# Kernel tuning notes

Hardware: AMD Instinct MI355X
Metric: run time of the kernel (lower is better)

The kernel has to match this reference:

```python
import jax, jax.numpy as jnp
import numpy as np

B, T, D_MODEL = 2, 2048, 2048
NH, NKV, DH = 16, 4, 128
N_REP = NH // NKV
NV = 256  # n_vision_tokens
THETA = 10000.0
NEG = -1e9


def setup_inputs() -> dict:
    key = jax.random.key(0)
    ks = jax.random.split(key, 5)
    x = jax.random.normal(ks[0], (B, T, D_MODEL), jnp.float32)
    # rope_freqs = exp(i * t * theta^{-2j/D}) represented as cos/sin, shape [T, DH//2]
    inv = 1.0 / (THETA ** (np.arange(0, DH, 2, dtype=np.float64) / DH))
    ang = np.outer(np.arange(T, dtype=np.float64), inv)
    cos = jnp.asarray(np.cos(ang), jnp.float32)
    sin = jnp.asarray(np.sin(ang), jnp.float32)
    sc = 0.02
    wq = jax.random.normal(ks[1], (D_MODEL, NH * DH), jnp.float32) * sc
    wk = jax.random.normal(ks[2], (D_MODEL, NKV * DH), jnp.float32) * sc
    wv = jax.random.normal(ks[3], (D_MODEL, NKV * DH), jnp.float32) * sc
    wo = jax.random.normal(ks[4], (NH * DH, D_MODEL), jnp.float32) * sc
    return {"x": x, "cos": cos, "sin": sin, "wq": wq, "wk": wk, "wv": wv,
            "wo": wo, "n_vision_tokens": NV}


def _rope(t, cos, sin):
    # t: [B,H,L,D]; pairs (even=real, odd=imag); cos/sin: [L, D//2]
    a = t[..., 0::2]
    b = t[..., 1::2]
    c = cos[None, None]
    s = sin[None, None]
    ra = a * c - b * s
    rb = a * s + b * c
    return jnp.stack([ra, rb], axis=-1).reshape(t.shape)


def reference(x, cos, sin, wq, wk, wv, wo, n_vision_tokens):
    Bx, Tx, _ = x.shape
    nv = int(n_vision_tokens)
    tl = Tx - nv  # text length

    q = (x @ wq).reshape(Bx, Tx, NH, DH).transpose(0, 2, 1, 3)   # [B,NH,T,DH]
    k = (x @ wk).reshape(Bx, Tx, NKV, DH).transpose(0, 2, 1, 3)  # [B,NKV,T,DH]
    v = (x @ wv).reshape(Bx, Tx, NKV, DH).transpose(0, 2, 1, 3)

    # RoPE only on the text portion (vision tokens keep raw q/k)
    c, s = cos[:tl], sin[:tl]
    q = jnp.concatenate([q[:, :, :nv], _rope(q[:, :, nv:], c, s)], axis=2)
    k = jnp.concatenate([k[:, :, :nv], _rope(k[:, :, nv:], c, s)], axis=2)

    new_kv_cache = (k, v)

    # GQA: repeat_interleave KV heads
    k = jnp.repeat(k, N_REP, axis=1)
    v = jnp.repeat(v, N_REP, axis=1)

    attn = jnp.einsum('bhqd,bhkd->bhqk', q, k) / jnp.sqrt(jnp.float32(DH))

    # hybrid mask: vision rows/cols fully visible; text-text strictly causal
    text_mask = jnp.triu(jnp.ones((tl, tl), bool), k=1)
    mask = jnp.zeros((Tx, Tx), bool).at[nv:, nv:].set(text_mask)
    attn = jnp.where(mask[None, None], NEG, attn)

    attn = jax.nn.softmax(attn, axis=-1)
    out = jnp.einsum('bhqk,bhkd->bhqd', attn, v)
    out = out.transpose(0, 2, 1, 3).reshape(Bx, Tx, NH * DH) @ wo
    return out, new_kv_cache
```

## Files before the change

### kernel.cpp

```cpp
#include <hip/hip_runtime.h>
#include <hip/hip_bf16.h>

#define BB 2
#define TT 2048
#define DMODEL 2048
#define NH 16
#define NKV 4
#define DH 128
#define NV 256
#define TL (TT - NV)
#define NQKV 3072

typedef __bf16  bf16x8  __attribute__((ext_vector_type(8)));
typedef float   float4v __attribute__((ext_vector_type(4)));
typedef short   short8  __attribute__((ext_vector_type(8)));
typedef unsigned short ushort;

__device__ __forceinline__ float bf2f(ushort u) {
    union { float f; unsigned i; } c; c.i = ((unsigned)u) << 16; return c.f;
}
__device__ __forceinline__ ushort f2bf(float f) {
    union { float f; unsigned i; } c; c.f = f;
    unsigned r = c.i + 0x7fff + ((c.i >> 16) & 1);
    return (ushort)(r >> 16);
}
__device__ __forceinline__ unsigned cvtpk(float a, float b) {
    unsigned r;
    asm("v_cvt_pk_bf16_f32 %0, %1, %2" : "=v"(r) : "v"(a), "v"(b));
    return r;
}

#define GLDS16(g, l) __builtin_amdgcn_global_load_lds( \
    (__attribute__((address_space(1))) void*)(g), \
    (__attribute__((address_space(3))) void*)(l), 16, 0, 0)

#define NJOB 51
#define NSLOT 19
#define WOJOBS 64
__device__ const short J_QT[NJOB] = {
    16,  0, 0, 1, 1, 2, 2, 3, 3, 31, 31, 30, 15,
    30, 29, 29, 28, 14, 28, 27, 27, 26, 13, 26, 25, 25, 24, 12,
    24, 23, 23, 22, 11, 22, 21, 21, 20, 10, 20, 19, 19, 18,  9,
    18, 17, 17,  8,  7,  6,  5,  4 };
__device__ const short J_K0[NJOB] = {
     0,  0,16, 0,16, 0,16, 0,16,  0, 16,  0,  0,
    16,  0,15, 0,  0, 15,  0, 14,  0,  0, 14,  0, 13,  0,  0,
    13,  0,12, 0,  0, 12,  0, 11,  0,  0, 11,  0, 10,  0,  0,
    10,  0, 9, 0,  0,  0,  0,  0 };
__device__ const short J_K1[NJOB] = {
    17, 16,32,16,32,16,32,16,32, 16, 32, 16, 16,
    31, 15,30,15, 15, 29, 14, 28, 14, 14, 27, 13, 26, 13, 13,
    25, 12,24,12, 12, 23, 11, 22, 11, 11, 21, 10, 20, 10, 10,
    19,  9,18, 9,  8,  7,  6,  5 };
__device__ const short J_PH[NJOB] = {
   255,  0, 1, 2, 3, 4, 5, 6, 7, 36, 37, 34,255,
    35, 32,33,30,255, 31, 28, 29, 26,255, 27, 24, 25, 22,255,
    23, 20,21,18,255, 19, 16, 17, 14,255, 15, 12, 13, 10,255,
    11,  8, 9,255,255,255,255,255 };

__global__ __launch_bounds__(256) void prep(
    const float* __restrict__ x, ushort* __restrict__ xbf,
    const float* __restrict__ wq, const float* __restrict__ wk,
    const float* __restrict__ wv, ushort* __restrict__ wT)
{
    __shared__ ushort st[64][72];
    int bid = blockIdx.x;
    if (bid < 4096) {
        size_t i = ((size_t)bid * 256 + threadIdx.x) * 8;
        float4v f0 = *(const float4v*)&x[i];
        float4v f1 = *(const float4v*)&x[i + 4];
        short8 h;
        h[0] = (short)f2bf(f0[0]); h[1] = (short)f2bf(f0[1]);
        h[2] = (short)f2bf(f0[2]); h[3] = (short)f2bf(f0[3]);
        h[4] = (short)f2bf(f1[0]); h[5] = (short)f2bf(f1[1]);
        h[6] = (short)f2bf(f1[2]); h[7] = (short)f2bf(f1[3]);
        *(short8*)&xbf[i] = h;
        return;
    }
    bid -= 4096;
    int bx = bid % 48, by = bid / 48;
    int n0 = bx * 64, k0 = by * 64;
    const float* w; int N, nn;
    if (n0 < 2048)      { w = wq; N = 2048; nn = n0; }
    else if (n0 < 2560) { w = wk; N = 512;  nn = n0 - 2048; }
    else                { w = wv; N = 512;  nn = n0 - 2560; }
    int r  = threadIdx.x >> 2;
    int c0 = (threadIdx.x & 3) * 16;
    #pragma unroll
    for (int j = 0; j < 16; j += 4) {
        float4v f = *(const float4v*)&w[(size_t)(k0 + r) * N + nn + c0 + j];
        st[c0 + j + 0][r] = f2bf(f[0]);
        st[c0 + j + 1][r] = f2bf(f[1]);
        st[c0 + j + 2][r] = f2bf(f[2]);
        st[c0 + j + 3][r] = f2bf(f[3]);
    }
    __syncthreads();
    ushort* dst = &wT[(size_t)(n0 + r) * DMODEL + k0];
    *(short8*)&dst[c0]     = *(short8*)&st[r][c0];
    *(short8*)&dst[c0 + 8] = *(short8*)&st[r][c0 + 8];
}

#define RQ_BLOCKS 14336
#define RK_BLOCKS 4096
__global__ __launch_bounds__(256) void postproc(
    ushort* __restrict__ qkv,
    const float* __restrict__ cosp, const float* __restrict__ sinp,
    float* __restrict__ kout, float* __restrict__ vout,
    ushort* __restrict__ kbf, ushort* __restrict__ vbfT)
{
    __shared__ ushort st[64][72];
    int bid = blockIdx.x;
    if (bid < RQ_BLOCKS) {
        int b   = bid / (RQ_BLOCKS / 2);
        int idx = (bid % (RQ_BLOCKS / 2)) * 256 + threadIdx.x;
        int i  = idx & 63;
        int h  = (idx >> 6) & 15;
        int tr = idx >> 10;
        int t  = NV + tr;
        size_t off = ((size_t)(b * TT + t)) * NQKV + h * DH + 2 * i;
        unsigned pk = *(const unsigned*)&qkv[off];
        float a  = bf2f((ushort)(pk & 0xffff));
        float bb = bf2f((ushort)(pk >> 16));
        float c  = cosp[tr * 64 + i];
        float s  = sinp[tr * 64 + i];
        *(unsigned*)&qkv[off] = cvtpk(a * c - bb * s, a * s + bb * c);
        return;
    }
    bid -= RQ_BLOCKS;
    if (bid < RK_BLOCKS) {
        int idx = bid * 256 + threadIdx.x;
        int i  = idx & 63;
        int kh = (idx >> 6) & 3;
        int t  = (idx >> 8) & 2047;
        int b  = idx >> 19;
        size_t row = ((size_t)(b * TT + t)) * NQKV;
        size_t dst = ((size_t)((b * NKV + kh) * TT + t)) * DH + 2 * i;
        unsigned pk = *(const unsigned*)&qkv[row + 2048 + kh * DH + 2 * i];
        float ka = bf2f((ushort)(pk & 0xffff));
        float kb = bf2f((ushort)(pk >> 16));
        if (t >= NV) {
            int pos = t - NV;
            float c = cosp[pos * 64 + i];
            float s = sinp[pos * 64 + i];
            float ra = ka * c - kb * s;
            float rb = ka * s + kb * c;
            ka = ra; kb = rb;
        }
        kout[dst]     = ka;
        kout[dst + 1] = kb;
        *(unsigned*)&kbf[dst] = cvtpk(ka, kb);
        unsigned pv = *(const unsigned*)&qkv[row + 2560 + kh * DH + 2 * i];
        vout[dst]     = bf2f((ushort)(pv & 0xffff));
        vout[dst + 1] = bf2f((ushort)(pv >> 16));
        return;
    }
    bid -= RK_BLOCKS;
    {
        int bx = bid & 31, by = (bid >> 5) & 1, bk = bid >> 6;
        int t0 = bx * 64, d0 = by * 64;
        int b = bk >> 2, kh = bk & 3;
        int r  = threadIdx.x >> 2;
        int c0 = (threadIdx.x & 3) * 16;
        const ushort* src = qkv + ((size_t)(b * TT + t0 + r)) * NQKV + 2560 + kh * DH + d0;
        short8 a0 = *(const short8*)&src[c0];
        short8 a1 = *(const short8*)&src[c0 + 8];
        #pragma unroll
        for (int j = 0; j < 8; j++) {
            st[c0 + j][r]     = (ushort)a0[j];
            st[c0 + 8 + j][r] = (ushort)a1[j];
        }
        __syncthreads();
        ushort* dst = vbfT + ((size_t)(bk * DH + d0 + r)) * TT + t0;
        *(short8*)&dst[c0]     = *(short8*)&st[r][c0];
        *(short8*)&dst[c0 + 8] = *(short8*)&st[r][c0 + 8];
    }
}

__global__ __launch_bounds__(256) void gemm_lds(
    const ushort* __restrict__ A, int lda,
    const ushort* __restrict__ BT,
    ushort* __restrict__ C, int ldc, int K)
{
    __shared__ ushort As[2][128 * 32];
    __shared__ ushort Bs[2][128 * 32];

    int tid = threadIdx.x;
    int wave = tid >> 6, lane = tid & 63, quad = lane >> 4, l16 = lane & 15;

    int nwg = gridDim.x * gridDim.y;
    int bid = blockIdx.x + gridDim.x * blockIdx.y;
    int cpx = nwg >> 3;
    int swz = (bid & 7) * cpx + (bid >> 3);
    int bx = swz % gridDim.x, by = swz / gridDim.x;
    int m0 = by * 128, n0 = bx * 128;
    int wr = (wave >> 1) * 64, wc = (wave & 1) * 64;

    int srow = tid >> 2, scol = (tid & 3) * 8;
    const ushort* ag = A  + (size_t)(m0 + srow) * lda + scol;
    const ushort* bg = BT + (size_t)(n0 + srow) * K   + scol;
    int lo0 = (wave * 16) * 32;
    int lo1 = (64 + wave * 16) * 32;

    float4v acc[4][4];
    for (int i = 0; i < 4; i++)
        for (int j = 0; j < 4; j++)
            acc[i][j] = (float4v){0.f, 0.f, 0.f, 0.f};

    auto stage = [&](int buf, int k0) {
        GLDS16(ag + k0,                    As[buf] + lo0);
        GLDS16(ag + (size_t)64 * lda + k0, As[buf] + lo1);
        GLDS16(bg + k0,                    Bs[buf] + lo0);
        GLDS16(bg + (size_t)64 * K + k0,   Bs[buf] + lo1);
    };

    stage(0, 0);
    int it = 0;
    for (int k0 = 0; k0 < K; k0 += 32, ++it) {
        int cur = it & 1;
        __syncthreads();
        if (k0 + 32 < K) stage(cur ^ 1, k0 + 32);

        bf16x8 af[4], bfr[4];
        #pragma unroll
        for (int i = 0; i < 4; i++) af[i] = *(const bf16x8*)&As[cur][(wr + i * 16 + l16) * 32 + quad * 8];
        #pragma unroll
        for (int j = 0; j < 4; j++) bfr[j] = *(const bf16x8*)&Bs[cur][(wc + j * 16 + l16) * 32 + quad * 8];
        #pragma unroll
        for (int i = 0; i < 4; i++)
            #pragma unroll
            for (int j = 0; j < 4; j++)
                acc[i][j] = __builtin_amdgcn_mfma_f32_16x16x32_bf16(af[i], bfr[j], acc[i][j], 0, 0, 0);
    }

    #pragma unroll
    for (int i = 0; i < 4; i++)
        #pragma unroll
        for (int j = 0; j < 4; j++)
            #pragma unroll
            for (int r = 0; r < 4; r++) {
                int row = m0 + wr + i * 16 + quad * 4 + r;
                int col = n0 + wc + j * 16 + l16;
                C[(size_t)row * ldc + col] = f2bf(acc[i][j][r]);
            }
}

__global__ __launch_bounds__(256) void gemm_out(
    const ushort* __restrict__ A,
    const ushort* __restrict__ Bc,
    float* __restrict__ C)
{
    __shared__ ushort As[2][128 * 32];
    __shared__ ushort Bs[2][128 * 32];

    int tid = threadIdx.x;
    int wave = tid >> 6, lane = tid & 63, quad = lane >> 4, l16 = lane & 15;

    int nwg = gridDim.x * gridDim.y;
    int bid = blockIdx.x + gridDim.x * blockIdx.y;
    int cpx = nwg >> 3;
    int swz = (bid & 7) * cpx + (bid >> 3);
    int bx = swz % gridDim.x, by = swz / gridDim.x;
    int m0 = by * 128, n0 = bx * 128;
    int wr = (wave >> 1) * 64, wc = (wave & 1) * 64;

    int srow = tid >> 2, scol = (tid & 3) * 8;
    const ushort* ag = A  + (size_t)(m0 + srow) * NQKV + scol;
    const ushort* bg = Bc + (size_t)(n0 + srow) * 6144 + scol;
    int lo0 = (wave * 16) * 32;
    int lo1 = (64 + wave * 16) * 32;

    float4v acc[4][4];
    for (int i = 0; i < 4; i++)
        for (int j = 0; j < 4; j++)
            acc[i][j] = (float4v){0.f, 0.f, 0.f, 0.f};

    auto stage = [&](int buf, int k0) {
        int koff = ((k0 >> 10) * NQKV) + (k0 & 1023);
        GLDS16(ag + k0,                       As[buf] + lo0);
        GLDS16(ag + (size_t)64 * NQKV + k0,   As[buf] + lo1);
        GLDS16(bg + koff,                     Bs[buf] + lo0);
        GLDS16(bg + (size_t)64 * 6144 + koff, Bs[buf] + lo1);
    };

    stage(0, 0);
    int it = 0;
    for (int k0 = 0; k0 < 2048; k0 += 32, ++it) {
        int cur = it & 1;
        __syncthreads();
        if (k0 + 32 < 2048) stage(cur ^ 1, k0 + 32);

        bf16x8 af[4], bfr[4];
        #pragma unroll
        for (int i = 0; i < 4; i++) af[i] = *(const bf16x8*)&As[cur][(wr + i * 16 + l16) * 32 + quad * 8];
        #pragma unroll
        for (int j = 0; j < 4; j++) bfr[j] = *(const bf16x8*)&Bs[cur][(wc + j * 16 + l16) * 32 + quad * 8];
        #pragma unroll
        for (int i = 0; i < 4; i++)
            #pragma unroll
            for (int j = 0; j < 4; j++)
                acc[i][j] = __builtin_amdgcn_mfma_f32_16x16x32_bf16(af[i], bfr[j], acc[i][j], 0, 0, 0);
    }

    #pragma unroll
    for (int i = 0; i < 4; i++)
        #pragma unroll
        for (int j = 0; j < 4; j++)
            #pragma unroll
            for (int r = 0; r < 4; r++) {
                int row = m0 + wr + i * 16 + quad * 4 + r;
                int col = n0 + wc + j * 16 + l16;
                C[(size_t)row * DMODEL + col] = acc[i][j][r];
            }
}

__global__ __launch_bounds__(256, 2) void attn_kernel(
    ushort* qkv,
    const ushort* __restrict__ kbf, const ushort* __restrict__ vbfT,
    ushort* __restrict__ pO, float* __restrict__ ml,
    const float* __restrict__ wo)
{
    __shared__ ushort shm[40960];

    int tid = threadIdx.x;
    int hy = blockIdx.x;
    int b  = blockIdx.y;
    int zz = blockIdx.z;

    if (zz >= NJOB) {
        int idx = (zz - NJOB) * 16 + b * 8 + hy;
        int n0 = (idx & 31) * 64, k0 = (idx >> 5) * 64;
        ushort (*st)[72] = (ushort(*)[72])shm;
        int r  = tid >> 2;
        int c0 = (tid & 3) * 16;
        #pragma unroll
        for (int j = 0; j < 16; j += 4) {
            float4v f = *(const float4v*)&wo[(size_t)(k0 + r) * DMODEL + n0 + c0 + j];
            st[c0 + j + 0][r] = f2bf(f[0]);
            st[c0 + j + 1][r] = f2bf(f[1]);
            st[c0 + j + 2][r] = f2bf(f[2]);
            st[c0 + j + 3][r] = f2bf(f[3]);
        }
        __syncthreads();
        ushort* dst = qkv + ((size_t)(2 * (n0 + r) + (k0 >> 10))) * NQKV + 2048 + (k0 & 1023);
        *(short8*)&dst[c0]     = *(short8*)&st[r][c0];
        *(short8*)&dst[c0 + 8] = *(short8*)&st[r][c0 + 8];
        return;
    }

    int job = zz;
    int wave = tid >> 6, lane = tid & 63, quad = lane >> 4, l16 = lane & 15;
    int qt  = J_QT[job];
    int kt0 = J_K0[job];
    int kt1 = J_K1[job];
    int ph  = J_PH[job];
    int h0 = hy * 2;
    int kh = hy >> 1;
    int q0 = qt * 64;

    int srow = tid >> 2, scol = (tid & 3) * 8;

    ushort* qbase0 = qkv + ((size_t)(b * TT) + q0) * NQKV + h0 * DH;
    ushort* qbase1 = qbase0 + DH;
    #pragma unroll
    for (int dk = 0; dk < 4; dk++) {
        GLDS16(qbase0 + (size_t)srow * NQKV + dk * 32 + scol, shm + dk * 2048 + wave * 512);
        GLDS16(qbase1 + (size_t)srow * NQKV + dk * 32 + scol, shm + 16384 + dk * 2048 + wave * 512);
    }
    __syncthreads();
    bf16x8 qf0[4], qf1[4];
    #pragma unroll
    for (int dk = 0; dk < 4; dk++) {
        qf0[dk] = *(const bf16x8*)&shm[dk * 2048 + (wave * 16 + l16) * 32 + quad * 8];
        qf1[dk] = *(const bf16x8*)&shm[16384 + dk * 2048 + (wave * 16 + l16) * 32 + quad * 8];
    }
    __syncthreads();

    float4v O0[8], O1[8];
    #pragma unroll
    for (int i = 0; i < 8; i++) {
        O0[i] = (float4v){0.f, 0.f, 0.f, 0.f};
        O1[i] = (float4v){0.f, 0.f, 0.f, 0.f};
    }
    float m0r = -1e30f, l0r = 0.f;
    float m1r = -1e30f, l1r = 0.f;

    const float scale = 0.08838834764831845f;
    const float THRR  = 90.50966799f;
    int qg = q0 + wave * 16 + l16;

    const ushort* kb2 = kbf  + ((size_t)(b * NKV + kh)) * TT * DH;
    const ushort* vb2 = vbfT + ((size_t)(b * NKV + kh)) * DH * TT;

    ushort* Pl = shm + 32768 + wave * 2048;
    int qsw = l16 & 7;

    auto stage = [&](int buf, int kt) {
        ushort* Kb = shm + buf * 16384;
        ushort* Vb = Kb + 8192;
        int k0 = kt * 64;
        #pragma unroll
        for (int dk = 0; dk < 4; dk++)
            GLDS16(kb2 + (size_t)(k0 + srow) * DH + dk * 32 + scol, Kb + dk * 2048 + wave * 512);
        #pragma unroll
        for (int kk = 0; kk < 2; kk++)
            #pragma unroll
            for (int p = 0; p < 2; p++)
                GLDS16(vb2 + (size_t)(p * 64 + srow) * TT + k0 + kk * 32 + scol,
                       Vb + kk * 4096 + (p * 64 + wave * 16) * 32);
    };

    stage(0, kt0);

    for (int kt = kt0; kt < kt1; kt++) {
        int cur = (kt - kt0) & 1;
        __syncthreads();
        if (kt + 1 < kt1)
            stage(cur ^ 1, kt + 1);

        const ushort* Kc = shm + cur * 16384;
        const ushort* Vc = Kc + 8192;
        int k0 = kt * 64;

        float4v s0[4], s1[4];
        __builtin_amdgcn_s_setprio(1);
        #pragma unroll
        for (int t2i = 0; t2i < 4; t2i++) {
            float4v a0 = (float4v){0.f, 0.f, 0.f, 0.f};
            float4v a1 = (float4v){0.f, 0.f, 0.f, 0.f};
            #pragma unroll
            for (int dk = 0; dk < 4; dk++) {
                bf16x8 af = *(const bf16x8*)&Kc[dk * 2048 + (t2i * 16 + l16) * 32 + quad * 8];
                a0 = __builtin_amdgcn_mfma_f32_16x16x32_bf16(af, qf0[dk], a0, 0, 0, 0);
                a1 = __builtin_amdgcn_mfma_f32_16x16x32_bf16(af, qf1[dk], a1, 0, 0, 0);
            }
            s0[t2i] = a0; s1[t2i] = a1;
        }
        __builtin_amdgcn_s_setprio(0);

        if ((q0 >= NV) && (kt == qt)) {
            #pragma unroll
            for (int t2i = 0; t2i < 4; t2i++)
                #pragma unroll
                for (int i = 0; i < 4; i++)
                    if (k0 + t2i * 16 + quad * 4 + i > qg) {
                        s0[t2i][i] = -1e9f;
                        s1[t2i][i] = -1e9f;
                    }
        }

        float mx0 = -1e30f, mx1 = -1e30f;
        #pragma unroll
        for (int t2i = 0; t2i < 4; t2i++)
            #pragma unroll
            for (int i = 0; i < 4; i++) {
                mx0 = fmaxf(mx0, s0[t2i][i]);
                mx1 = fmaxf(mx1, s1[t2i][i]);
            }
        mx0 = fmaxf(mx0, __shfl_xor(mx0, 16, 64));
        mx0 = fmaxf(mx0, __shfl_xor(mx0, 32, 64));
        mx1 = fmaxf(mx1, __shfl_xor(mx1, 16, 64));
        mx1 = fmaxf(mx1, __shfl_xor(mx1, 32, 64));

        bool skip0 = __all(mx0 <= m0r + THRR);
        bool skip1 = __all(mx1 <= m1r + THRR);
        float mn0 = fmaxf(m0r, mx0), mn1 = fmaxf(m1r, mx1);
        float mref0 = skip0 ? m0r : mn0;
        float mref1 = skip1 ? m1r : mn1;
        float nb0 = -mref0 * scale;
        float nb1 = -mref1 * scale;

        float ss0 = 0.f, ss1 = 0.f;
        #pragma unroll
        for (int t2i = 0; t2i < 4; t2i++)
            #pragma unroll
            for (int i = 0; i < 4; i++) {
                float p0 = __expf(__builtin_fmaf(s0[t2i][i], scale, nb0)); s0[t2i][i] = p0; ss0 += p0;
                float p1 = __expf(__builtin_fmaf(s1[t2i][i], scale, nb1)); s1[t2i][i] = p1; ss1 += p1;
            }
        ss0 += __shfl_xor(ss0, 16, 64); ss0 += __shfl_xor(ss0, 32, 64);
        ss1 += __shfl_xor(ss1, 16, 64); ss1 += __shfl_xor(ss1, 32, 64);

        if (!skip0) {
            float al0 = __expf((m0r - mn0) * scale);
            #pragma unroll
            for (int dt = 0; dt < 8; dt++)
                #pragma unroll
                for (int i = 0; i < 4; i++) O0[dt][i] *= al0;
            l0r *= al0;
            m0r = mn0;
        }
        l0r += ss0;
        if (!skip1) {
            float al1 = __expf((m1r - mn1) * scale);
            #pragma unroll
            for (int dt = 0; dt < 8; dt++)
                #pragma unroll
                for (int i = 0; i < 4; i++) O1[dt][i] *= al1;
            l1r *= al1;
            m1r = mn1;
        }
        l1r += ss1;

        #pragma unroll
        for (int t2i = 0; t2i < 4; t2i++) {
            int g = t2i * 2 + (quad >> 1);
            int base = l16 * 64 + ((g ^ qsw) << 3) + (quad & 1) * 4;
            *(unsigned*)&Pl[base]            = cvtpk(s0[t2i][0], s0[t2i][1]);
            *(unsigned*)&Pl[base + 2]        = cvtpk(s0[t2i][2], s0[t2i][3]);
            *(unsigned*)&Pl[1024 + base]     = cvtpk(s1[t2i][0], s1[t2i][1]);
            *(unsigned*)&Pl[1024 + base + 2] = cvtpk(s1[t2i][2], s1[t2i][3]);
        }

        #pragma unroll
        for (int kk = 0; kk < 2; kk++) {
            int gc = kk * 4 + quad;
            int raddr = l16 * 64 + ((gc ^ qsw) << 3);
            bf16x8 pf0 = *(const bf16x8*)&Pl[raddr];
            bf16x8 pf1 = *(const bf16x8*)&Pl[1024 + raddr];
            __builtin_amdgcn_s_setprio(1);
            #pragma unroll
            for (int dt = 0; dt < 8; dt++) {
                bf16x8 vf = *(const bf16x8*)&Vc[kk * 4096 + (dt * 16 + l16) * 32 + quad * 8];
                O0[dt] = __builtin_amdgcn_mfma_f32_16x16x32_bf16(vf, pf0, O0[dt], 0, 0, 0);
                O1[dt] = __builtin_amdgcn_mfma_f32_16x16x32_bf16(vf, pf1, O1[dt], 0, 0, 0);
            }
            __builtin_amdgcn_s_setprio(0);
        }
    }

    float rinv0 = 1.f / l0r, rinv1 = 1.f / l1r;
    int qrow = wave * 16 + l16;
    if (ph == 255 || (ph & 1)) {
        size_t orow = (size_t)qrow * NQKV;
        #pragma unroll
        for (int dt = 0; dt < 8; dt++)
            #pragma unroll
            for (int i = 0; i < 4; i += 2) {
                unsigned pk0 = cvtpk(O0[dt][i] * rinv0, O0[dt][i + 1] * rinv0);
                unsigned pk1 = cvtpk(O1[dt][i] * rinv1, O1[dt][i + 1] * rinv1);
                *(unsigned*)&qbase0[orow + dt * 16 + quad * 4 + i] = pk0;
                *(unsigned*)&qbase1[orow + dt * 16 + quad * 4 + i] = pk1;
            }
    } else {
        int g = ((b * 8 + hy) * NSLOT) + (ph >> 1);
        ushort* pb = pO + (size_t)g * 16384 + qrow * 256;
        #pragma unroll
        for (int dt = 0; dt < 8; dt++)
            #pragma unroll
            for (int i = 0; i < 4; i += 2) {
                int d = dt * 16 + quad * 4 + i;
                *(unsigned*)&pb[d]       = cvtpk(O0[dt][i] * rinv0, O0[dt][i + 1] * rinv0);
                *(unsigned*)&pb[128 + d] = cvtpk(O1[dt][i] * rinv1, O1[dt][i + 1] * rinv1);
            }
    }
    if (ph != 255 && quad == 0) {
        int g = ((b * 8 + hy) * NSLOT) + (ph >> 1);
        int half = ph & 1;
        float* mlb = ml + (size_t)g * 512 + half * 256 + qrow * 2;
        mlb[0]   = m0r;  mlb[1]   = l0r;
        mlb[128] = m1r;  mlb[129] = l1r;
    }
}

__global__ __launch_bounds__(256) void combine_split(
    ushort* __restrict__ qkv, const ushort* __restrict__ pO,
    const float* __restrict__ ml)
{
    int g = blockIdx.x;
    int slice = g / NSLOT, local = g % NSLOT;
    int b = slice >> 3, hy = slice & 7;
    int qt = (local < 4) ? local : (13 + local);
    int h0 = hy * 2;
    int q0 = qt * 64;

    int t = threadIdx.x;
    int r = t >> 2, seg = t & 3;
    int head = seg >> 1;
    const float scale = 0.08838834764831845f;

    const float* mlg = ml + (size_t)g * 512;
    float m0 = mlg[0 * 256 + head * 128 + r * 2];
    float l0 = mlg[0 * 256 + head * 128 + r * 2 + 1];
    float m1 = mlg[1 * 256 + head * 128 + r * 2];
    float l1 = mlg[1 * 256 + head * 128 + r * 2 + 1];
    float mm = fmaxf(m0, m1);
    float w0 = __expf((m0 - mm) * scale) * l0;
    float w1 = __expf((m1 - mm) * scale) * l1;
    float inv = 1.f / (w0 + w1);
    float a0 = w0 * inv, a1 = w1 * inv;

    const ushort* p = pO + (size_t)g * 16384 + r * 256 + seg * 64;
    ushort* q = qkv + ((size_t)(b * TT + q0 + r)) * NQKV + (h0 + head) * DH + (seg & 1) * 64;

    #pragma unroll
    for (int j = 0; j < 64; j += 2) {
        unsigned u0 = *(const unsigned*)&p[j];
        unsigned u1 = *(const unsigned*)&q[j];
        float lo = bf2f((ushort)(u0 & 0xffff)) * a0 + bf2f((ushort)(u1 & 0xffff)) * a1;
        float hi2 = bf2f((ushort)(u0 >> 16)) * a0 + bf2f((ushort)(u1 >> 16)) * a1;
        *(unsigned*)&q[j] = cvtpk(lo, hi2);
    }
}

extern "C" void kernel_launch(void* const* d_in, const int* in_sizes, int n_in,
                              void* d_out, int out_size, void* d_ws, size_t ws_size,
                              hipStream_t stream) {
    const float* x    = (const float*)d_in[0];
    const float* cosp = (const float*)d_in[1];
    const float* sinp = (const float*)d_in[2];
    const float* wq   = (const float*)d_in[3];
    const float* wk   = (const float*)d_in[4];
    const float* wv   = (const float*)d_in[5];
    const float* wo   = (const float*)d_in[6];

    float* out  = (float*)d_out;
    float* kout = out + (size_t)BB * TT * DMODEL;
    float* vout = kout + (size_t)BB * NKV * TT * DH;

    ushort* sc    = (ushort*)d_out;
    ushort* wqkvT = sc;
    ushort* xbf   = sc + (size_t)NQKV * DMODEL;
    ushort* kbf   = sc + (size_t)NQKV * DMODEL;
    ushort* vbfT  = kbf + (size_t)BB * NKV * TT * DH;
    ushort* pO    = sc;
    float*  ml    = (float*)(sc + 15000000);

    ushort* qkv = (ushort*)d_ws;

    const int M = BB * TT;

    prep<<<dim3(4096 + 1536), 256, 0, stream>>>(x, xbf, wq, wk, wv, wqkvT);

    gemm_lds<<<dim3(NQKV / 128, M / 128), 256, 0, stream>>>(
        xbf, DMODEL, wqkvT, qkv, NQKV, DMODEL);

    postproc<<<dim3(RQ_BLOCKS + RK_BLOCKS + 512), 256, 0, stream>>>(
        qkv, cosp, sinp, kout, vout, kbf, vbfT);

    attn_kernel<<<dim3(NH / 2, BB, NJOB + WOJOBS), 256, 0, stream>>>(
        qkv, kbf, vbfT, pO, ml, wo);

    combine_split<<<dim3(16 * NSLOT), 256, 0, stream>>>(qkv, pO, ml);

    gemm_out<<<dim3(DMODEL / 128, M / 128), 256, 0, stream>>>(qkv, qkv + 2048, out);
}
```

Baseline: 342.7 us.

## Process all four GQA query heads per block sharing K/V tiles, vectorize postproc

The attention kernel now uses 512-thread blocks that cover all four query heads of one KV head. Each K/V tile staged in LDS is therefore reused by 8 waves instead of 4, which halves K/V global traffic. The split-K job schedule, the partial-output and ml layouts, and the combine kernel are reworked to match, and the Wo transpose jobs are packed two per block. The postproc RoPE and K/V conversion paths now handle 8 elements per thread with vector loads and stores. The trade-offs are fewer blocks, a higher register and occupancy target (launch bounds of 512 threads, 4 blocks), and more LDS traffic for the P matrix.

```diff
diff --git a/kernel.cpp b/kernel.cpp
--- a/kernel.cpp
+++ b/kernel.cpp
@@ -34,29 +34,29 @@
     (__attribute__((address_space(1))) void*)(g), \
     (__attribute__((address_space(3))) void*)(l), 16, 0, 0)
 
-#define NJOB 51
-#define NSLOT 19
+#define NJOB 52
+#define NSLOT 20
 #define WOJOBS 64
 __device__ const short J_QT[NJOB] = {
-    16,  0, 0, 1, 1, 2, 2, 3, 3, 31, 31, 30, 15,
-    30, 29, 29, 28, 14, 28, 27, 27, 26, 13, 26, 25, 25, 24, 12,
-    24, 23, 23, 22, 11, 22, 21, 21, 20, 10, 20, 19, 19, 18,  9,
-    18, 17, 17,  8,  7,  6,  5,  4 };
+     0,  0,  1,  1,  2,  2,  3,  3, 30, 31, 31, 15,
+    28, 29, 29, 30, 14, 26, 27, 27, 28, 13, 24, 25, 25, 26, 12,
+    22, 23, 23, 24, 11, 20, 21, 21, 22, 10, 18, 19, 19, 20,  9,
+    16, 17, 17, 18,  8, 16,  7,  6,  5,  4 };
 __device__ const short J_K0[NJOB] = {
-     0,  0,16, 0,16, 0,16, 0,16,  0, 16,  0,  0,
-    16,  0,15, 0,  0, 15,  0, 14,  0,  0, 14,  0, 13,  0,  0,
-    13,  0,12, 0,  0, 12,  0, 11,  0,  0, 11,  0, 10,  0,  0,
-    10,  0, 9, 0,  0,  0,  0,  0 };
+     0, 16,  0, 16,  0, 16,  0, 16, 15,  0, 16,  0,
+    14,  0, 15,  0,  0, 13,  0, 14,  0,  0, 12,  0, 13,  0,  0,
+    11,  0, 12,  0,  0, 10,  0, 11,  0,  0,  9,  0, 10,  0,  0,
+     8,  0,  9,  0,  0,  0,  0,  0,  0,  0 };
 __device__ const short J_K1[NJOB] = {
-    17, 16,32,16,32,16,32,16,32, 16, 32, 16, 16,
-    31, 15,30,15, 15, 29, 14, 28, 14, 14, 27, 13, 26, 13, 13,
-    25, 12,24,12, 12, 23, 11, 22, 11, 11, 21, 10, 20, 10, 10,
-    19,  9,18, 9,  8,  7,  6,  5 };
+    16, 32, 16, 32, 16, 32, 16, 32, 31, 16, 32, 16,
+    29, 15, 30, 15, 15, 27, 14, 28, 14, 14, 25, 13, 26, 13, 13,
+    23, 12, 24, 12, 12, 21, 11, 22, 11, 11, 19, 10, 20, 10, 10,
+    17,  9, 18,  9,  9,  8,  8,  7,  6,  5 };
 __device__ const short J_PH[NJOB] = {
-   255,  0, 1, 2, 3, 4, 5, 6, 7, 36, 37, 34,255,
-    35, 32,33,30,255, 31, 28, 29, 26,255, 27, 24, 25, 22,255,
-    23, 20,21,18,255, 19, 16, 17, 14,255, 15, 12, 13, 10,255,
-    11,  8, 9,255,255,255,255,255 };
+     0,  1,  2,  3,  4,  5,  6,  7, 37, 38, 39, 255,
+    33, 34, 35, 36, 255, 29, 30, 31, 32, 255, 25, 26, 27, 28, 255,
+    21, 22, 23, 24, 255, 17, 18, 19, 20, 255, 13, 14, 15, 16, 255,
+     9, 10, 11, 12, 255,  8, 255, 255, 255, 255 };
 
 __global__ __launch_bounds__(256) void prep(
     const float* __restrict__ x, ushort* __restrict__ xbf,
@@ -100,8 +100,8 @@
     *(short8*)&dst[c0 + 8] = *(short8*)&st[r][c0 + 8];
 }
 
-#define RQ_BLOCKS 14336
-#define RK_BLOCKS 4096
+#define RQ_BLOCKS 3584
+#define RK_BLOCKS 1024
 __global__ __launch_bounds__(256) void postproc(
     ushort* __restrict__ qkv,
     const float* __restrict__ cosp, const float* __restrict__ sinp,
@@ -111,47 +111,69 @@
     __shared__ ushort st[64][72];
     int bid = blockIdx.x;
     if (bid < RQ_BLOCKS) {
-        int b   = bid / (RQ_BLOCKS / 2);
-        int idx = (bid % (RQ_BLOCKS / 2)) * 256 + threadIdx.x;
-        int i  = idx & 63;
-        int h  = (idx >> 6) & 15;
-        int tr = idx >> 10;
-        int t  = NV + tr;
-        size_t off = ((size_t)(b * TT + t)) * NQKV + h * DH + 2 * i;
-        unsigned pk = *(const unsigned*)&qkv[off];
-        float a  = bf2f((ushort)(pk & 0xffff));
-        float bb = bf2f((ushort)(pk >> 16));
-        float c  = cosp[tr * 64 + i];
-        float s  = sinp[tr * 64 + i];
-        *(unsigned*)&qkv[off] = cvtpk(a * c - bb * s, a * s + bb * c);
+        int idx = bid * 256 + threadIdx.x;
+        int i4 = idx & 15;
+        int h  = (idx >> 4) & 15;
+        int tr = idx >> 8;
+        int b  = tr >= TL;
+        int trr = tr - b * TL;
+        size_t off = ((size_t)(b * TT + NV + trr)) * NQKV + h * DH + i4 * 8;
+        short8 v = *(const short8*)&qkv[off];
+        float4v c4 = *(const float4v*)&cosp[trr * 64 + i4 * 4];
+        float4v s4 = *(const float4v*)&sinp[trr * 64 + i4 * 4];
+        short8 o;
+        #pragma unroll
+        for (int p = 0; p < 4; p++) {
+            float a  = bf2f((ushort)v[2 * p]);
+            float bb = bf2f((ushort)v[2 * p + 1]);
+            unsigned pk = cvtpk(a * c4[p] - bb * s4[p], a * s4[p] + bb * c4[p]);
+            o[2 * p]     = (short)(pk & 0xffff);
+            o[2 * p + 1] = (short)(pk >> 16);
+        }
+        *(short8*)&qkv[off] = o;
         return;
     }
     bid -= RQ_BLOCKS;
     if (bid < RK_BLOCKS) {
         int idx = bid * 256 + threadIdx.x;
-        int i  = idx & 63;
-        int kh = (idx >> 6) & 3;
-        int t  = (idx >> 8) & 2047;
-        int b  = idx >> 19;
+        int i4 = idx & 15;
+        int kh = (idx >> 4) & 3;
+        int t  = (idx >> 6) & 2047;
+        int b  = idx >> 17;
         size_t row = ((size_t)(b * TT + t)) * NQKV;
-        size_t dst = ((size_t)((b * NKV + kh) * TT + t)) * DH + 2 * i;
-        unsigned pk = *(const unsigned*)&qkv[row + 2048 + kh * DH + 2 * i];
-        float ka = bf2f((ushort)(pk & 0xffff));
-        float kb = bf2f((ushort)(pk >> 16));
+        size_t dst = ((size_t)((b * NKV + kh) * TT + t)) * DH + i4 * 8;
+        short8 kv = *(const short8*)&qkv[row + 2048 + kh * DH + i4 * 8];
+        short8 vv = *(const short8*)&qkv[row + 2560 + kh * DH + i4 * 8];
+        float kf[8];
+        #pragma unroll
+        for (int p = 0; p < 8; p++) kf[p] = bf2f((ushort)kv[p]);
         if (t >= NV) {
             int pos = t - NV;
-            float c = cosp[pos * 64 + i];
-            float s = sinp[pos * 64 + i];
-            float ra = ka * c - kb * s;
-            float rb = ka * s + kb * c;
-            ka = ra; kb = rb;
-        }
-        kout[dst]     = ka;
-        kout[dst + 1] = kb;
-        *(unsigned*)&kbf[dst] = cvtpk(ka, kb);
-        unsigned pv = *(const unsigned*)&qkv[row + 2560 + kh * DH + 2 * i];
-        vout[dst]     = bf2f((ushort)(pv & 0xffff));
-        vout[dst + 1] = bf2f((ushort)(pv >> 16));
+            float4v c4 = *(const float4v*)&cosp[pos * 64 + i4 * 4];
+            float4v s4 = *(const float4v*)&sinp[pos * 64 + i4 * 4];
+            #pragma unroll
+            for (int p = 0; p < 4; p++) {
+                float ra = kf[2 * p] * c4[p] - kf[2 * p + 1] * s4[p];
+                float rb = kf[2 * p] * s4[p] + kf[2 * p + 1] * c4[p];
+                kf[2 * p] = ra; kf[2 * p + 1] = rb;
+            }
+        }
+        float4v ko0 = {kf[0], kf[1], kf[2], kf[3]};
+        float4v ko1 = {kf[4], kf[5], kf[6], kf[7]};
+        *(float4v*)&kout[dst]     = ko0;
+        *(float4v*)&kout[dst + 4] = ko1;
+        short8 kb8;
+        #pragma unroll
+        for (int p = 0; p < 4; p++) {
+            unsigned pk = cvtpk(kf[2 * p], kf[2 * p + 1]);
+            kb8[2 * p]     = (short)(pk & 0xffff);
+            kb8[2 * p + 1] = (short)(pk >> 16);
+        }
+        *(short8*)&kbf[dst] = kb8;
+        float4v vo0 = {bf2f((ushort)vv[0]), bf2f((ushort)vv[1]), bf2f((ushort)vv[2]), bf2f((ushort)vv[3])};
+        float4v vo1 = {bf2f((ushort)vv[4]), bf2f((ushort)vv[5]), bf2f((ushort)vv[6]), bf2f((ushort)vv[7])};
+        *(float4v*)&vout[dst]     = vo0;
+        *(float4v*)&vout[dst + 4] = vo1;
         return;
     }
     bid -= RK_BLOCKS;
@@ -313,7 +335,7 @@
             }
 }
 
-__global__ __launch_bounds__(256, 2) void attn_kernel(
+__global__ __launch_bounds__(512, 4) void attn_kernel(
     ushort* qkv,
     const ushort* __restrict__ kbf, const ushort* __restrict__ vbfT,
     ushort* __restrict__ pO, float* __restrict__ ml,
@@ -322,16 +344,16 @@
     __shared__ ushort shm[40960];
 
     int tid = threadIdx.x;
-    int hy = blockIdx.x;
-    int b  = blockIdx.y;
-    int zz = blockIdx.z;
+    int kh = blockIdx.x >> 1, b = blockIdx.x & 1;
+    int zz = blockIdx.y;
 
     if (zz >= NJOB) {
-        int idx = (zz - NJOB) * 16 + b * 8 + hy;
+        int half = tid >> 8, tid2 = tid & 255;
+        int idx = (zz - NJOB) * 16 + blockIdx.x * 2 + half;
         int n0 = (idx & 31) * 64, k0 = (idx >> 5) * 64;
-        ushort (*st)[72] = (ushort(*)[72])shm;
-        int r  = tid >> 2;
-        int c0 = (tid & 3) * 16;
+        ushort (*st)[72] = (ushort(*)[72])(shm + half * 4608);
+        int r  = tid2 >> 2;
+        int c0 = (tid2 & 3) * 16;
         #pragma unroll
         for (int j = 0; j < 16; j += 4) {
             float4v f = *(const float4v*)&wo[(size_t)(k0 + r) * DMODEL + n0 + c0 + j];
@@ -349,29 +371,29 @@
 
     int job = zz;
     int wave = tid >> 6, lane = tid & 63, quad = lane >> 4, l16 = lane & 15;
+    int pair = wave >> 2, wv = wave & 3;
     int qt  = J_QT[job];
     int kt0 = J_K0[job];
     int kt1 = J_K1[job];
     int ph  = J_PH[job];
-    int h0 = hy * 2;
-    int kh = hy >> 1;
     int q0 = qt * 64;
 
-    int srow = tid >> 2, scol = (tid & 3) * 8;
-
-    ushort* qbase0 = qkv + ((size_t)(b * TT) + q0) * NQKV + h0 * DH;
-    ushort* qbase1 = qbase0 + DH;
+    int lr = lane >> 2, lc = (lane & 3) * 8;
+
     #pragma unroll
-    for (int dk = 0; dk < 4; dk++) {
-        GLDS16(qbase0 + (size_t)srow * NQKV + dk * 32 + scol, shm + dk * 2048 + wave * 512);
-        GLDS16(qbase1 + (size_t)srow * NQKV + dk * 32 + scol, shm + 16384 + dk * 2048 + wave * 512);
+    for (int j = 0; j < 8; j++) {
+        int t = wave * 8 + j;
+        int g = t >> 4, r = t & 15, dk = r >> 2, rg = r & 3;
+        const ushort* qb = qkv + ((size_t)(b * TT) + q0 + rg * 16 + lr) * NQKV
+                         + (kh * 4 + g) * DH + dk * 32 + lc;
+        GLDS16(qb, shm + g * 8192 + dk * 2048 + rg * 512);
     }
     __syncthreads();
     bf16x8 qf0[4], qf1[4];
     #pragma unroll
     for (int dk = 0; dk < 4; dk++) {
-        qf0[dk] = *(const bf16x8*)&shm[dk * 2048 + (wave * 16 + l16) * 32 + quad * 8];
-        qf1[dk] = *(const bf16x8*)&shm[16384 + dk * 2048 + (wave * 16 + l16) * 32 + quad * 8];
+        qf0[dk] = *(const bf16x8*)&shm[(pair * 2 + 0) * 8192 + dk * 2048 + (wv * 16 + l16) * 32 + quad * 8];
+        qf1[dk] = *(const bf16x8*)&shm[(pair * 2 + 1) * 8192 + dk * 2048 + (wv * 16 + l16) * 32 + quad * 8];
     }
     __syncthreads();
 
@@ -386,12 +408,12 @@
 
     const float scale = 0.08838834764831845f;
     const float THRR  = 90.50966799f;
-    int qg = q0 + wave * 16 + l16;
+    int qg = q0 + wv * 16 + l16;
 
     const ushort* kb2 = kbf  + ((size_t)(b * NKV + kh)) * TT * DH;
     const ushort* vb2 = vbfT + ((size_t)(b * NKV + kh)) * DH * TT;
 
-    ushort* Pl = shm + 32768 + wave * 2048;
+    ushort* Pl = shm + 32768 + wave * 1024;
     int qsw = l16 & 7;
 
     auto stage = [&](int buf, int kt) {
@@ -399,14 +421,19 @@
         ushort* Vb = Kb + 8192;
         int k0 = kt * 64;
         #pragma unroll
-        for (int dk = 0; dk < 4; dk++)
-            GLDS16(kb2 + (size_t)(k0 + srow) * DH + dk * 32 + scol, Kb + dk * 2048 + wave * 512);
-        #pragma unroll
-        for (int kk = 0; kk < 2; kk++)
-            #pragma unroll
-            for (int p = 0; p < 2; p++)
-                GLDS16(vb2 + (size_t)(p * 64 + srow) * TT + k0 + kk * 32 + scol,
-                       Vb + kk * 4096 + (p * 64 + wave * 16) * 32);
+        for (int j = 0; j < 4; j++) {
+            int t = wave * 4 + j;
+            if (t < 16) {
+                int dk = t >> 2, rg = t & 3;
+                GLDS16(kb2 + (size_t)(k0 + rg * 16 + lr) * DH + dk * 32 + lc,
+                       Kb + dk * 2048 + rg * 512);
+            } else {
+                int t2 = t - 16;
+                int kk = t2 >> 3, p2 = (t2 >> 2) & 1, rg = t2 & 3;
+                GLDS16(vb2 + (size_t)(p2 * 64 + rg * 16 + lr) * TT + k0 + kk * 32 + lc,
+                       Vb + kk * 4096 + p2 * 2048 + rg * 512);
+            }
+        }
     };
 
     stage(0, kt0);
@@ -501,35 +528,49 @@
         }
         l1r += ss1;
 
+        bf16x8 pf0[2], pf1[2];
         #pragma unroll
         for (int t2i = 0; t2i < 4; t2i++) {
             int g = t2i * 2 + (quad >> 1);
             int base = l16 * 64 + ((g ^ qsw) << 3) + (quad & 1) * 4;
-            *(unsigned*)&Pl[base]            = cvtpk(s0[t2i][0], s0[t2i][1]);
-            *(unsigned*)&Pl[base + 2]        = cvtpk(s0[t2i][2], s0[t2i][3]);
-            *(unsigned*)&Pl[1024 + base]     = cvtpk(s1[t2i][0], s1[t2i][1]);
-            *(unsigned*)&Pl[1024 + base + 2] = cvtpk(s1[t2i][2], s1[t2i][3]);
-        }
-
+            *(unsigned*)&Pl[base]     = cvtpk(s0[t2i][0], s0[t2i][1]);
+            *(unsigned*)&Pl[base + 2] = cvtpk(s0[t2i][2], s0[t2i][3]);
+        }
         #pragma unroll
         for (int kk = 0; kk < 2; kk++) {
             int gc = kk * 4 + quad;
-            int raddr = l16 * 64 + ((gc ^ qsw) << 3);
-            bf16x8 pf0 = *(const bf16x8*)&Pl[raddr];
-            bf16x8 pf1 = *(const bf16x8*)&Pl[1024 + raddr];
+            pf0[kk] = *(const bf16x8*)&Pl[l16 * 64 + ((gc ^ qsw) << 3)];
+        }
+        #pragma unroll
+        for (int t2i = 0; t2i < 4; t2i++) {
+            int g = t2i * 2 + (quad >> 1);
+            int base = l16 * 64 + ((g ^ qsw) << 3) + (quad & 1) * 4;
+            *(unsigned*)&Pl[base]     = cvtpk(s1[t2i][0], s1[t2i][1]);
+            *(unsigned*)&Pl[base + 2] = cvtpk(s1[t2i][2], s1[t2i][3]);
+        }
+        #pragma unroll
+        for (int kk = 0; kk < 2; kk++) {
+            int gc = kk * 4 + quad;
+            pf1[kk] = *(const bf16x8*)&Pl[l16 * 64 + ((gc ^ qsw) << 3)];
+        }
+
+        #pragma unroll
+        for (int kk = 0; kk < 2; kk++) {
             __builtin_amdgcn_s_setprio(1);
             #pragma unroll
             for (int dt = 0; dt < 8; dt++) {
                 bf16x8 vf = *(const bf16x8*)&Vc[kk * 4096 + (dt * 16 + l16) * 32 + quad * 8];
-                O0[dt] = __builtin_amdgcn_mfma_f32_16x16x32_bf16(vf, pf0, O0[dt], 0, 0, 0);
-                O1[dt] = __builtin_amdgcn_mfma_f32_16x16x32_bf16(vf, pf1, O1[dt], 0, 0, 0);
+                O0[dt] = __builtin_amdgcn_mfma_f32_16x16x32_bf16(vf, pf0[kk], O0[dt], 0, 0, 0);
+                O1[dt] = __builtin_amdgcn_mfma_f32_16x16x32_bf16(vf, pf1[kk], O1[dt], 0, 0, 0);
             }
             __builtin_amdgcn_s_setprio(0);
         }
     }
 
     float rinv0 = 1.f / l0r, rinv1 = 1.f / l1r;
-    int qrow = wave * 16 + l16;
+    int qrow = wv * 16 + l16;
+    ushort* qbase0 = qkv + ((size_t)(b * TT) + q0) * NQKV + (kh * 4 + pair * 2) * DH;
+    ushort* qbase1 = qbase0 + DH;
     if (ph == 255 || (ph & 1)) {
         size_t orow = (size_t)qrow * NQKV;
         #pragma unroll
@@ -542,8 +583,8 @@
                 *(unsigned*)&qbase1[orow + dt * 16 + quad * 4 + i] = pk1;
             }
     } else {
-        int g = ((b * 8 + hy) * NSLOT) + (ph >> 1);
-        ushort* pb = pO + (size_t)g * 16384 + qrow * 256;
+        int g = ((b * 4 + kh) * NSLOT) + (ph >> 1);
+        ushort* pb = pO + (size_t)g * 32768 + qrow * 512 + (pair * 2) * 128;
         #pragma unroll
         for (int dt = 0; dt < 8; dt++)
             #pragma unroll
@@ -554,9 +595,9 @@
             }
     }
     if (ph != 255 && quad == 0) {
-        int g = ((b * 8 + hy) * NSLOT) + (ph >> 1);
-        int half = ph & 1;
-        float* mlb = ml + (size_t)g * 512 + half * 256 + qrow * 2;
+        int g = ((b * 4 + kh) * NSLOT) + (ph >> 1);
+        int part = ph & 1;
+        float* mlb = ml + (size_t)g * 1024 + part * 512 + (pair * 2) * 128 + qrow * 2;
         mlb[0]   = m0r;  mlb[1]   = l0r;
         mlb[128] = m1r;  mlb[129] = l1r;
     }
@@ -567,37 +608,35 @@
     const float* __restrict__ ml)
 {
     int g = blockIdx.x;
-    int slice = g / NSLOT, local = g % NSLOT;
-    int b = slice >> 3, hy = slice & 7;
-    int qt = (local < 4) ? local : (13 + local);
-    int h0 = hy * 2;
+    int slice = g / NSLOT, slot = g % NSLOT;
+    int b = slice >> 2, kh = slice & 3;
+    int qt = (slot < 4) ? slot : (slot + 12);
     int q0 = qt * 64;
 
     int t = threadIdx.x;
-    int r = t >> 2, seg = t & 3;
-    int head = seg >> 1;
+    int r = t >> 2, hh = t & 3;
     const float scale = 0.08838834764831845f;
 
-    const float* mlg = ml + (size_t)g * 512;
-    float m0 = mlg[0 * 256 + head * 128 + r * 2];
-    float l0 = mlg[0 * 256 + head * 128 + r * 2 + 1];
-    float m1 = mlg[1 * 256 + head * 128 + r * 2];
-    float l1 = mlg[1 * 256 + head * 128 + r * 2 + 1];
+    const float* mlg = ml + (size_t)g * 1024;
+    float m0 = mlg[hh * 128 + r * 2];
+    float l0 = mlg[hh * 128 + r * 2 + 1];
+    float m1 = mlg[512 + hh * 128 + r * 2];
+    float l1 = mlg[512 + hh * 128 + r * 2 + 1];
     float mm = fmaxf(m0, m1);
     float w0 = __expf((m0 - mm) * scale) * l0;
     float w1 = __expf((m1 - mm) * scale) * l1;
     float inv = 1.f / (w0 + w1);
     float a0 = w0 * inv, a1 = w1 * inv;
 
-    const ushort* p = pO + (size_t)g * 16384 + r * 256 + seg * 64;
-    ushort* q = qkv + ((size_t)(b * TT + q0 + r)) * NQKV + (h0 + head) * DH + (seg & 1) * 64;
+    const ushort* p = pO + (size_t)g * 32768 + r * 512 + hh * 128;
+    ushort* q = qkv + ((size_t)(b * TT + q0 + r)) * NQKV + (kh * 4 + hh) * DH;
 
     #pragma unroll
-    for (int j = 0; j < 64; j += 2) {
+    for (int j = 0; j < 128; j += 2) {
         unsigned u0 = *(const unsigned*)&p[j];
         unsigned u1 = *(const unsigned*)&q[j];
-        float lo = bf2f((ushort)(u0 & 0xffff)) * a0 + bf2f((ushort)(u1 & 0xffff)) * a1;
-        float hi2 = bf2f((ushort)(u0 >> 16)) * a0 + bf2f((ushort)(u1 >> 16)) * a1;
+        float lo  = bf2f((ushort)(u0 & 0xffff)) * a0 + bf2f((ushort)(u1 & 0xffff)) * a1;
+        float hi2 = bf2f((ushort)(u0 >> 16))    * a0 + bf2f((ushort)(u1 >> 16))    * a1;
         *(unsigned*)&q[j] = cvtpk(lo, hi2);
     }
 }
@@ -637,10 +676,10 @@
     postproc<<<dim3(RQ_BLOCKS + RK_BLOCKS + 512), 256, 0, stream>>>(
         qkv, cosp, sinp, kout, vout, kbf, vbfT);
 
-    attn_kernel<<<dim3(NH / 2, BB, NJOB + WOJOBS), 256, 0, stream>>>(
+    attn_kernel<<<dim3(8, NJOB + WOJOBS), 512, 0, stream>>>(
         qkv, kbf, vbfT, pO, ml, wo);
 
-    combine_split<<<dim3(16 * NSLOT), 256, 0, stream>>>(qkv, pO, ml);
+    combine_split<<<dim3(8 * NSLOT), 256, 0, stream>>>(qkv, pO, ml);
 
     gemm_out<<<dim3(DMODEL / 128, M / 128), 256, 0, stream>>>(qkv, qkv + 2048, out);
 }
```

Result: slower. 450.1 us (+31.4%).
